# Kernel tuning notes

Measured on AMD Instinct MI355X. Metric: run time of the kernel, lower is better.

Reference implementation:

```python
import jax, jax.numpy as jnp
import numpy as np

HIDDEN = 1024
INTER = 4096
EPS = 1e-12


def _ste(q, x):
    # straight-through estimator: forward q, backward identity wrt x
    return x + jax.lax.stop_gradient(q - x)


def setup_inputs() -> dict:
    key = jax.random.key(0)
    ks = jax.random.split(key, 4)
    hidden_states = jax.random.normal(ks[0], (4, 2048, INTER), dtype=jnp.float32)
    input_tensor = jax.random.normal(ks[1], (4, 2048, HIDDEN), dtype=jnp.float32)
    W = jax.random.normal(ks[2], (HIDDEN, INTER), dtype=jnp.float32) * 0.02
    b = jnp.zeros((HIDDEN,), dtype=jnp.float32)
    clip_val = jnp.asarray(2.5, dtype=jnp.float32)  # learnable elastic alpha
    gamma = jnp.ones((HIDDEN,), dtype=jnp.float32)
    beta = jnp.zeros((HIDDEN,), dtype=jnp.float32)
    return {"hidden_states": hidden_states, "input_tensor": input_tensor,
            "W": W, "b": b, "clip_val": clip_val, "gamma": gamma, "beta": beta}


def reference(hidden_states, input_tensor, W, b, clip_val, gamma, beta):
    # --- binary weight (BWN): per-output-channel scale = mean(|W|, axis=in) ---
    w_scale = jnp.mean(jnp.abs(W), axis=1, keepdims=True)  # [hidden, 1]
    W_q = _ste(w_scale * jnp.sign(W), W)                    # [hidden, inter]
    # --- elastic signed binary activation: q = alpha * sign(x / alpha) ---
    s = hidden_states / clip_val
    x_q = clip_val * _ste(jnp.sign(s), s)                   # [b, s, inter]
    # --- dense projection ---
    h = jnp.einsum('bsi,hi->bsh', x_q, W_q) + b             # [b, s, hidden]
    # dropout prob 0.0 (eval mode) -> no-op
    # --- residual + LayerNorm (eps=1e-12) ---
    r = h + input_tensor
    mu = jnp.mean(r, axis=-1, keepdims=True)
    var = jnp.mean(jnp.square(r - mu), axis=-1, keepdims=True)
    out = (r - mu) * jax.lax.rsqrt(var + EPS) * gamma + beta
    return out
```

## Files before the change

kernel.cpp:

```cpp
#include <hip/hip_runtime.h>
#include <stdint.h>

#define HIDDEN 1024
#define INTER  4096
#define ROWS   8192
#define BM     32
#define BN     512
#define NKSTEP 64
#define NBLK   512
#define BSTEP  65536

typedef int i32x4 __attribute__((ext_vector_type(4)));

__device__ __forceinline__ uint32_t sgn4(float4 v) {
    uint32_t b0 = (v.x < 0.f) ? 0xFFu : 0x01u;
    uint32_t b1 = (v.y < 0.f) ? 0xFFu : 0x01u;
    uint32_t b2 = (v.z < 0.f) ? 0xFFu : 0x01u;
    uint32_t b3 = (v.w < 0.f) ? 0xFFu : 0x01u;
    return b0 | (b1 << 8) | (b2 << 16) | (b3 << 24);
}

__global__ __launch_bounds__(256)
void pack_w_kernel(const float* __restrict__ W, uint8_t* __restrict__ Bg,
                   float* __restrict__ wscale) {
    int h = blockIdx.x;
    int tid = threadIdx.x;
    int lane = tid & 63, wv = tid >> 6;
    const float4* row = (const float4*)(W + (size_t)h * INTER);
    const uint32_t base_h = (uint32_t)(h >> 4) * 1024u + (uint32_t)(h & 15) * 16u;
    float asum = 0.f;
    #pragma unroll
    for (int q = 0; q < 4; ++q) {
        int g = q * 256 + tid;
        float4 v = row[g];
        asum += fabsf(v.x) + fabsf(v.y) + fabsf(v.z) + fabsf(v.w);
        uint32_t off = (uint32_t)(g >> 4) * (uint32_t)BSTEP + base_h
                     + (uint32_t)((g & 15) >> 2) * 256u + (uint32_t)(g & 3) * 4u;
        *(uint32_t*)(Bg + off) = sgn4(v);
    }
    #pragma unroll
    for (int off = 32; off > 0; off >>= 1) asum += __shfl_down(asum, off);
    __shared__ float red[4];
    if (lane == 0) red[wv] = asum;
    __syncthreads();
    if (tid == 0) wscale[h] = (red[0] + red[1] + red[2] + red[3]) * (1.0f / INTER);
}

__global__ __launch_bounds__(512, 4)
void gemm_kernel(const float* __restrict__ hs, const float* __restrict__ input,
                 const float* __restrict__ bias, const float* __restrict__ clipp,
                 float* __restrict__ out, const uint8_t* __restrict__ Bg,
                 const float* __restrict__ wscale, float2* __restrict__ sqws) {
    __shared__ alignas(16) uint8_t yls[65536];
    __shared__ alignas(16) uint8_t sA[2 * 2048];

    const int tid  = threadIdx.x;
    const int lane = tid & 63;
    const int wave = tid >> 6;
    const int mt   = blockIdx.x & 255;
    const int ch   = blockIdx.x >> 8;
    const int m0   = mt * BM;

    const int r  = tid >> 4;
    const int c4 = tid & 15;
    const int awofs = (r >> 4) * 1024 + ((c4 >> 2) * 16 + (r & 15)) * 16 + (c4 & 3) * 4;
    const float* aload = hs + (size_t)(m0 + r) * INTER + c4 * 4;

    const uint8_t* bbase = Bg + (size_t)(ch * 32 + wave * 4) * 1024 + lane * 16;
    const int fofs = lane * 16;

    i32x4 acc[2][4];
    #pragma unroll
    for (int rt = 0; rt < 2; ++rt)
        #pragma unroll
        for (int cf = 0; cf < 4; ++cf) acc[rt][cf] = (i32x4){0, 0, 0, 0};
    i32x4 Bb0[4], Bb1[4];

    float4 avA = *(const float4*)aload;
    #pragma unroll
    for (int cf = 0; cf < 4; ++cf) Bb0[cf] = *(const i32x4*)(bbase + cf * 1024);
    *(uint32_t*)&sA[awofs] = sgn4(avA);
    avA = *(const float4*)(aload + 64);
    asm volatile("s_waitcnt lgkmcnt(0)" ::: "memory");
    __builtin_amdgcn_s_barrier();

#define BODY(T, CUR, BC, BN_, PFB, PFA) do {                                   \
    i32x4 af0_ = *(const i32x4*)&sA[(CUR) * 2048 + fofs];                      \
    i32x4 af1_ = *(const i32x4*)&sA[(CUR) * 2048 + 1024 + fofs];               \
    if (PFB) {                                                                 \
        const uint8_t* bp_ = bbase + (size_t)((T) + 1) * BSTEP;                \
        _Pragma("unroll")                                                      \
        for (int cf_ = 0; cf_ < 4; ++cf_)                                      \
            Bb##BN_[cf_] = *(const i32x4*)(bp_ + cf_ * 1024);                  \
    }                                                                          \
    __builtin_amdgcn_s_setprio(1);                                             \
    _Pragma("unroll")                                                          \
    for (int cf_ = 0; cf_ < 4; ++cf_) {                                        \
        acc[0][cf_] = __builtin_amdgcn_mfma_i32_16x16x64_i8(af0_, Bb##BC[cf_], acc[0][cf_], 0, 0, 0); \
        acc[1][cf_] = __builtin_amdgcn_mfma_i32_16x16x64_i8(af1_, Bb##BC[cf_], acc[1][cf_], 0, 0, 0); \
    }                                                                          \
    __builtin_amdgcn_s_setprio(0);                                             \
    if (PFB) {                                                                 \
        *(uint32_t*)&sA[((CUR) ^ 1) * 2048 + awofs] = sgn4(avA);               \
        if (PFA) avA = *(const float4*)(aload + ((T) + 2) * 64);               \
        asm volatile("s_waitcnt lgkmcnt(0)" ::: "memory");                     \
        __builtin_amdgcn_s_barrier();                                          \
    }                                                                          \
} while (0)

    for (int tt = 0; tt < 31; ++tt) {
        BODY(2 * tt,     0, 0, 1, 1, 1);
        BODY(2 * tt + 1, 1, 1, 0, 1, 1);
    }
    BODY(62, 0, 0, 1, 1, 0);
    BODY(63, 1, 1, 0, 0, 0);
#undef BODY

    const float clip = clipp[0];
    const int l15 = lane & 15;
    const int g4i = lane >> 4;
    float cw[4], bi[4];
    #pragma unroll
    for (int cf = 0; cf < 4; ++cf) {
        int gcol = ch * BN + wave * 64 + cf * 16 + l15;
        cw[cf] = clip * wscale[gcol];
        bi[cf] = bias[gcol];
    }
    float* yl = (float*)yls;
    #pragma unroll
    for (int rt = 0; rt < 2; ++rt)
        #pragma unroll
        for (int cf = 0; cf < 4; ++cf)
            #pragma unroll
            for (int rg = 0; rg < 4; ++rg) {
                int rw = rt * 16 + g4i * 4 + rg;
                int cl = wave * 64 + cf * 16 + l15;
                yl[rw * BN + cl] = fmaf((float)acc[rt][cf][rg], cw[cf], bi[cf]);
            }
    __syncthreads();

    float4* yl4 = (float4*)yl;
    const float4* in4 = (const float4*)input;
    float4* out4 = (float4*)out;
    float s = 0.f, q = 0.f;
    #pragma unroll
    for (int j = 0; j < 8; ++j) {
        int idx  = r * 128 + c4 + j * 16;
        int gidx = (int)((size_t)0) + c4 + j * 16;
        float4 y4 = yl4[idx];
        float4 r4 = in4[(size_t)(m0 + r) * 256 + ch * 128 + gidx];
        y4.x += r4.x; y4.y += r4.y; y4.z += r4.z; y4.w += r4.w;
        out4[(size_t)(m0 + r) * 256 + ch * 128 + gidx] = y4;
        s += y4.x + y4.y + y4.z + y4.w;
        q += y4.x * y4.x + y4.y * y4.y + y4.z * y4.z + y4.w * y4.w;
    }
    #pragma unroll
    for (int off = 1; off <= 8; off <<= 1) {
        s += __shfl_xor(s, off);
        q += __shfl_xor(q, off);
    }
    if (c4 == 0) sqws[(size_t)(m0 + r) * 2 + ch] = make_float2(s, q);
}

__global__ __launch_bounds__(256)
void ln_kernel(float* __restrict__ out, const float2* __restrict__ sqws,
               const float* __restrict__ gamma, const float* __restrict__ beta) {
    const int lane = threadIdx.x & 63;
    const int wave = threadIdx.x >> 6;
    const int row  = blockIdx.x * 4 + wave;
    float2 p0 = sqws[(size_t)row * 2 + 0];
    float2 p1 = sqws[(size_t)row * 2 + 1];
    float ss = p0.x + p1.x, qq = p0.y + p1.y;
    float mu  = ss * (1.0f / HIDDEN);
    float var = fmaf(-mu, mu, qq * (1.0f / HIDDEN));
    float rs  = rsqrtf(var + 1e-12f);
    float4* rowp = (float4*)(out + (size_t)row * HIDDEN);
    const float4* gm4 = (const float4*)gamma;
    const float4* bt4 = (const float4*)beta;
    #pragma unroll
    for (int j = 0; j < 4; ++j) {
        int idx = lane + j * 64;
        float4 y = rowp[idx];
        float4 g = gm4[idx], b = bt4[idx];
        float4 o;
        o.x = (y.x - mu) * rs * g.x + b.x;
        o.y = (y.y - mu) * rs * g.y + b.y;
        o.z = (y.z - mu) * rs * g.z + b.z;
        o.w = (y.w - mu) * rs * g.w + b.w;
        rowp[idx] = o;
    }
}

extern "C" void kernel_launch(void* const* d_in, const int* in_sizes, int n_in,
                              void* d_out, int out_size, void* d_ws, size_t ws_size,
                              hipStream_t stream) {
    const float* hs    = (const float*)d_in[0];
    const float* inp   = (const float*)d_in[1];
    const float* W     = (const float*)d_in[2];
    const float* b     = (const float*)d_in[3];
    const float* clip  = (const float*)d_in[4];
    const float* gamma = (const float*)d_in[5];
    const float* beta  = (const float*)d_in[6];
    float* out = (float*)d_out;

    uint8_t* Bg   = (uint8_t*)d_ws;
    float* wscale = (float*)((char*)d_ws + 4u * 1024u * 1024u);
    float2* sqws  = (float2*)((char*)d_ws + 4u * 1024u * 1024u + 4096u);

    pack_w_kernel<<<HIDDEN, 256, 0, stream>>>(W, Bg, wscale);
    gemm_kernel<<<NBLK, 512, 0, stream>>>(hs, inp, b, clip, out, Bg, wscale, sqws);
    ln_kernel<<<ROWS / 4, 256, 0, stream>>>(out, sqws, gamma, beta);
}
```

Before: 298.3 us.

## Retile GEMM to 128x128 blocks and move row statistics into LayerNorm kernel

The GEMM block tile changes from 32x512 to 128x128. Each wave now owns one 16-column B fragment and eight 16-row A fragments, so each block reads much less of the packed weights per K step and shares sign-packed activations across more columns. The LDS staging of the output tile and the per-row partial sum and sum-of-squares are removed. The epilogue writes the scaled result plus residual straight to global memory, and the LayerNorm kernel recomputes the row statistics with a wave reduction over values it already keeps in registers. The trade-off is that epilogue stores are now strided scalar writes instead of coalesced float4 writes.

New measurement: 314.4 us. +5.4%, slower.

```diff
diff --git a/kernel.cpp b/kernel.cpp
--- a/kernel.cpp
+++ b/kernel.cpp
@@ -4,8 +4,8 @@
 #define HIDDEN 1024
 #define INTER  4096
 #define ROWS   8192
-#define BM     32
-#define BN     512
+#define BM     128
+#define BN     128
 #define NKSTEP 64
 #define NBLK   512
 #define BSTEP  65536
@@ -50,59 +50,78 @@
 void gemm_kernel(const float* __restrict__ hs, const float* __restrict__ input,
                  const float* __restrict__ bias, const float* __restrict__ clipp,
                  float* __restrict__ out, const uint8_t* __restrict__ Bg,
-                 const float* __restrict__ wscale, float2* __restrict__ sqws) {
-    __shared__ alignas(16) uint8_t yls[65536];
-    __shared__ alignas(16) uint8_t sA[2 * 2048];
+                 const float* __restrict__ wscale) {
+    __shared__ alignas(16) uint8_t sA[2 * 8192];
 
     const int tid  = threadIdx.x;
     const int lane = tid & 63;
     const int wave = tid >> 6;
-    const int mt   = blockIdx.x & 255;
-    const int ch   = blockIdx.x >> 8;
+    const int mt   = blockIdx.x & 63;
+    const int ch   = blockIdx.x >> 6;
     const int m0   = mt * BM;
 
-    const int r  = tid >> 4;
-    const int c4 = tid & 15;
-    const int awofs = (r >> 4) * 1024 + ((c4 >> 2) * 16 + (r & 15)) * 16 + (c4 & 3) * 4;
-    const float* aload = hs + (size_t)(m0 + r) * INTER + c4 * 4;
-
-    const uint8_t* bbase = Bg + (size_t)(ch * 32 + wave * 4) * 1024 + lane * 16;
+    const int r  = tid >> 2;
+    const int kc = tid & 3;
+    const int awofs = (r >> 4) * 1024 + (kc * 16 + (r & 15)) * 16;
+    const float* aload = hs + (size_t)(m0 + r) * INTER + kc * 16;
+
+    const uint8_t* bbase = Bg + (size_t)(ch * 8 + wave) * 1024 + lane * 16;
     const int fofs = lane * 16;
 
-    i32x4 acc[2][4];
-    #pragma unroll
-    for (int rt = 0; rt < 2; ++rt)
-        #pragma unroll
-        for (int cf = 0; cf < 4; ++cf) acc[rt][cf] = (i32x4){0, 0, 0, 0};
-    i32x4 Bb0[4], Bb1[4];
-
-    float4 avA = *(const float4*)aload;
-    #pragma unroll
-    for (int cf = 0; cf < 4; ++cf) Bb0[cf] = *(const i32x4*)(bbase + cf * 1024);
-    *(uint32_t*)&sA[awofs] = sgn4(avA);
-    avA = *(const float4*)(aload + 64);
+    i32x4 acc[8];
+    #pragma unroll
+    for (int rt = 0; rt < 8; ++rt) acc[rt] = (i32x4){0, 0, 0, 0};
+    i32x4 Bb0, Bb1;
+    float4 av0, av1, av2, av3;
+
+    av0 = *(const float4*)(aload + 0);
+    av1 = *(const float4*)(aload + 4);
+    av2 = *(const float4*)(aload + 8);
+    av3 = *(const float4*)(aload + 12);
+    Bb0 = *(const i32x4*)(bbase);
+    {
+        i32x4 sg = (i32x4){(int)sgn4(av0), (int)sgn4(av1),
+                           (int)sgn4(av2), (int)sgn4(av3)};
+        *(i32x4*)&sA[awofs] = sg;
+    }
+    av0 = *(const float4*)(aload + 64);
+    av1 = *(const float4*)(aload + 68);
+    av2 = *(const float4*)(aload + 72);
+    av3 = *(const float4*)(aload + 76);
     asm volatile("s_waitcnt lgkmcnt(0)" ::: "memory");
     __builtin_amdgcn_s_barrier();
 
 #define BODY(T, CUR, BC, BN_, PFB, PFA) do {                                   \
-    i32x4 af0_ = *(const i32x4*)&sA[(CUR) * 2048 + fofs];                      \
-    i32x4 af1_ = *(const i32x4*)&sA[(CUR) * 2048 + 1024 + fofs];               \
-    if (PFB) {                                                                 \
-        const uint8_t* bp_ = bbase + (size_t)((T) + 1) * BSTEP;                \
-        _Pragma("unroll")                                                      \
-        for (int cf_ = 0; cf_ < 4; ++cf_)                                      \
-            Bb##BN_[cf_] = *(const i32x4*)(bp_ + cf_ * 1024);                  \
-    }                                                                          \
+    const uint8_t* ab_ = sA + (CUR) * 8192;                                    \
+    i32x4 af0_ = *(const i32x4*)&ab_[0 * 1024 + fofs];                         \
+    i32x4 af1_ = *(const i32x4*)&ab_[1 * 1024 + fofs];                         \
+    i32x4 af2_ = *(const i32x4*)&ab_[2 * 1024 + fofs];                         \
+    i32x4 af3_ = *(const i32x4*)&ab_[3 * 1024 + fofs];                         \
+    i32x4 af4_ = *(const i32x4*)&ab_[4 * 1024 + fofs];                         \
+    i32x4 af5_ = *(const i32x4*)&ab_[5 * 1024 + fofs];                         \
+    i32x4 af6_ = *(const i32x4*)&ab_[6 * 1024 + fofs];                         \
+    i32x4 af7_ = *(const i32x4*)&ab_[7 * 1024 + fofs];                         \
+    if (PFB) Bb##BN_ = *(const i32x4*)(bbase + (size_t)((T) + 1) * BSTEP);     \
     __builtin_amdgcn_s_setprio(1);                                             \
-    _Pragma("unroll")                                                          \
-    for (int cf_ = 0; cf_ < 4; ++cf_) {                                        \
-        acc[0][cf_] = __builtin_amdgcn_mfma_i32_16x16x64_i8(af0_, Bb##BC[cf_], acc[0][cf_], 0, 0, 0); \
-        acc[1][cf_] = __builtin_amdgcn_mfma_i32_16x16x64_i8(af1_, Bb##BC[cf_], acc[1][cf_], 0, 0, 0); \
-    }                                                                          \
+    acc[0] = __builtin_amdgcn_mfma_i32_16x16x64_i8(af0_, Bb##BC, acc[0], 0, 0, 0); \
+    acc[1] = __builtin_amdgcn_mfma_i32_16x16x64_i8(af1_, Bb##BC, acc[1], 0, 0, 0); \
+    acc[2] = __builtin_amdgcn_mfma_i32_16x16x64_i8(af2_, Bb##BC, acc[2], 0, 0, 0); \
+    acc[3] = __builtin_amdgcn_mfma_i32_16x16x64_i8(af3_, Bb##BC, acc[3], 0, 0, 0); \
+    acc[4] = __builtin_amdgcn_mfma_i32_16x16x64_i8(af4_, Bb##BC, acc[4], 0, 0, 0); \
+    acc[5] = __builtin_amdgcn_mfma_i32_16x16x64_i8(af5_, Bb##BC, acc[5], 0, 0, 0); \
+    acc[6] = __builtin_amdgcn_mfma_i32_16x16x64_i8(af6_, Bb##BC, acc[6], 0, 0, 0); \
+    acc[7] = __builtin_amdgcn_mfma_i32_16x16x64_i8(af7_, Bb##BC, acc[7], 0, 0, 0); \
     __builtin_amdgcn_s_setprio(0);                                             \
     if (PFB) {                                                                 \
-        *(uint32_t*)&sA[((CUR) ^ 1) * 2048 + awofs] = sgn4(avA);               \
-        if (PFA) avA = *(const float4*)(aload + ((T) + 2) * 64);               \
+        i32x4 sg_ = (i32x4){(int)sgn4(av0), (int)sgn4(av1),                    \
+                            (int)sgn4(av2), (int)sgn4(av3)};                   \
+        *(i32x4*)&sA[((CUR) ^ 1) * 8192 + awofs] = sg_;                        \
+        if (PFA) {                                                             \
+            av0 = *(const float4*)(aload + ((T) + 2) * 64 + 0);                \
+            av1 = *(const float4*)(aload + ((T) + 2) * 64 + 4);                \
+            av2 = *(const float4*)(aload + ((T) + 2) * 64 + 8);                \
+            av3 = *(const float4*)(aload + ((T) + 2) * 64 + 12);               \
+        }                                                                      \
         asm volatile("s_waitcnt lgkmcnt(0)" ::: "memory");                     \
         __builtin_amdgcn_s_barrier();                                          \
     }                                                                          \
@@ -118,69 +137,53 @@
 
     const float clip = clipp[0];
     const int l15 = lane & 15;
-    const int g4i = lane >> 4;
-    float cw[4], bi[4];
-    #pragma unroll
-    for (int cf = 0; cf < 4; ++cf) {
-        int gcol = ch * BN + wave * 64 + cf * 16 + l15;
-        cw[cf] = clip * wscale[gcol];
-        bi[cf] = bias[gcol];
-    }
-    float* yl = (float*)yls;
-    #pragma unroll
-    for (int rt = 0; rt < 2; ++rt)
+    const int gcol = ch * BN + wave * 16 + l15;
+    const float cw = clip * wscale[gcol];
+    const float bi = bias[gcol];
+    const int rbase = (lane >> 4) * 4;
+    #pragma unroll
+    for (int rt = 0; rt < 8; ++rt) {
         #pragma unroll
-        for (int cf = 0; cf < 4; ++cf)
-            #pragma unroll
-            for (int rg = 0; rg < 4; ++rg) {
-                int rw = rt * 16 + g4i * 4 + rg;
-                int cl = wave * 64 + cf * 16 + l15;
-                yl[rw * BN + cl] = fmaf((float)acc[rt][cf][rg], cw[cf], bi[cf]);
-            }
-    __syncthreads();
-
-    float4* yl4 = (float4*)yl;
-    const float4* in4 = (const float4*)input;
-    float4* out4 = (float4*)out;
-    float s = 0.f, q = 0.f;
-    #pragma unroll
-    for (int j = 0; j < 8; ++j) {
-        int idx  = r * 128 + c4 + j * 16;
-        int gidx = (int)((size_t)0) + c4 + j * 16;
-        float4 y4 = yl4[idx];
-        float4 r4 = in4[(size_t)(m0 + r) * 256 + ch * 128 + gidx];
-        y4.x += r4.x; y4.y += r4.y; y4.z += r4.z; y4.w += r4.w;
-        out4[(size_t)(m0 + r) * 256 + ch * 128 + gidx] = y4;
-        s += y4.x + y4.y + y4.z + y4.w;
-        q += y4.x * y4.x + y4.y * y4.y + y4.z * y4.z + y4.w * y4.w;
-    }
-    #pragma unroll
-    for (int off = 1; off <= 8; off <<= 1) {
-        s += __shfl_xor(s, off);
-        q += __shfl_xor(q, off);
-    }
-    if (c4 == 0) sqws[(size_t)(m0 + r) * 2 + ch] = make_float2(s, q);
+        for (int rg = 0; rg < 4; ++rg) {
+            size_t gidx = (size_t)(m0 + rt * 16 + rbase + rg) * HIDDEN + gcol;
+            out[gidx] = fmaf((float)acc[rt][rg], cw, bi + input[gidx]);
+        }
+    }
 }
 
 __global__ __launch_bounds__(256)
-void ln_kernel(float* __restrict__ out, const float2* __restrict__ sqws,
-               const float* __restrict__ gamma, const float* __restrict__ beta) {
+void ln_kernel(float* __restrict__ out, const float* __restrict__ gamma,
+               const float* __restrict__ beta) {
     const int lane = threadIdx.x & 63;
     const int wave = threadIdx.x >> 6;
     const int row  = blockIdx.x * 4 + wave;
-    float2 p0 = sqws[(size_t)row * 2 + 0];
-    float2 p1 = sqws[(size_t)row * 2 + 1];
-    float ss = p0.x + p1.x, qq = p0.y + p1.y;
-    float mu  = ss * (1.0f / HIDDEN);
-    float var = fmaf(-mu, mu, qq * (1.0f / HIDDEN));
-    float rs  = rsqrtf(var + 1e-12f);
     float4* rowp = (float4*)(out + (size_t)row * HIDDEN);
     const float4* gm4 = (const float4*)gamma;
     const float4* bt4 = (const float4*)beta;
+
+    float4 v0 = rowp[lane +   0];
+    float4 v1 = rowp[lane +  64];
+    float4 v2 = rowp[lane + 128];
+    float4 v3 = rowp[lane + 192];
+    float s = v0.x + v0.y + v0.z + v0.w + v1.x + v1.y + v1.z + v1.w
+            + v2.x + v2.y + v2.z + v2.w + v3.x + v3.y + v3.z + v3.w;
+    float q = v0.x * v0.x + v0.y * v0.y + v0.z * v0.z + v0.w * v0.w
+            + v1.x * v1.x + v1.y * v1.y + v1.z * v1.z + v1.w * v1.w
+            + v2.x * v2.x + v2.y * v2.y + v2.z * v2.z + v2.w * v2.w
+            + v3.x * v3.x + v3.y * v3.y + v3.z * v3.z + v3.w * v3.w;
+    #pragma unroll
+    for (int off = 1; off < 64; off <<= 1) {
+        s += __shfl_xor(s, off);
+        q += __shfl_xor(q, off);
+    }
+    float mu  = s * (1.0f / HIDDEN);
+    float var = fmaf(-mu, mu, q * (1.0f / HIDDEN));
+    float rs  = rsqrtf(var + 1e-12f);
+
     #pragma unroll
     for (int j = 0; j < 4; ++j) {
         int idx = lane + j * 64;
-        float4 y = rowp[idx];
+        float4 y = (j == 0) ? v0 : (j == 1) ? v1 : (j == 2) ? v2 : v3;
         float4 g = gm4[idx], b = bt4[idx];
         float4 o;
         o.x = (y.x - mu) * rs * g.x + b.x;
@@ -205,9 +208,8 @@
 
     uint8_t* Bg   = (uint8_t*)d_ws;
     float* wscale = (float*)((char*)d_ws + 4u * 1024u * 1024u);
-    float2* sqws  = (float2*)((char*)d_ws + 4u * 1024u * 1024u + 4096u);
 
     pack_w_kernel<<<HIDDEN, 256, 0, stream>>>(W, Bg, wscale);
-    gemm_kernel<<<NBLK, 512, 0, stream>>>(hs, inp, b, clip, out, Bg, wscale, sqws);
-    ln_kernel<<<ROWS / 4, 256, 0, stream>>>(out, sqws, gamma, beta);
-}
+    gemm_kernel<<<NBLK, 512, 0, stream>>>(hs, inp, b, clip, out, Bg, wscale);
+    ln_kernel<<<ROWS / 4, 256, 0, stream>>>(out, gamma, beta);
+}
```
